# Kernel tuning notes

Measured on AMD Instinct MI355X. Metric: run time of the kernel, lower is better.

Reference implementation:

```python
import jax, jax.numpy as jnp
import numpy as np

B, N = 128, 64
HID, MLP, DS, DV = 128, 128, 32, 32
DH = MLP - DS - DV  # 64
FILL = -10.0


def _embed_mask(x, W, b, fill):
    # Linear+ReLU on non-NaN rows; fill NaN rows with `fill` (matches embed_with_masking).
    nan = jnp.isnan(x).any(-1)
    e = jax.nn.relu(jnp.where(jnp.isnan(x), 0.0, x) @ W + b)
    return jnp.where(nan[..., None], jnp.asarray(fill, x.dtype), e)


def setup_inputs() -> dict:
    key = jax.random.key(0)
    ks = jax.random.split(key, 12)
    s = 0.05
    return {
        "hidden_states": jax.random.normal(ks[0], (B, N, HID), jnp.float32),
        "obs1": jax.random.normal(ks[1], (B, N, 2), jnp.float32),
        "obs2": jax.random.normal(ks[2], (B, N, 2), jnp.float32),
        "w_sp": jax.random.normal(ks[3], (2, DS), jnp.float32) * s,
        "b_sp": jnp.zeros((DS,), jnp.float32),
        "w_vel": jax.random.normal(ks[4], (2, DV), jnp.float32) * s,
        "b_vel": jnp.zeros((DV,), jnp.float32),
        "w_hid": jax.random.normal(ks[5], (HID, DH), jnp.float32) * s,
        "b_hid": jnp.zeros((DH,), jnp.float32),
        "wq": jax.random.normal(ks[6], (MLP, MLP), jnp.float32) * s,
        "wk": jax.random.normal(ks[7], (MLP, MLP), jnp.float32) * s,
        "wv": jax.random.normal(ks[8], (MLP, MLP), jnp.float32) * s,
        "in_proj_w": jax.random.normal(ks[9], (MLP, 3 * MLP), jnp.float32) * s,
        "in_proj_b": jnp.zeros((3 * MLP,), jnp.float32),
        "mha_out_w": jax.random.normal(ks[10], (MLP, MLP), jnp.float32) * s,
        "mha_out_b": jnp.zeros((MLP,), jnp.float32),
        "out_w": jax.random.normal(ks[11], (MLP, MLP), jnp.float32) * s,
        "out_b": jnp.zeros((MLP,), jnp.float32),
    }


def reference(hidden_states, obs1, obs2, w_sp, b_sp, w_vel, b_vel, w_hid, b_hid,
              wq, wk, wv, in_proj_w, in_proj_b, mha_out_w, mha_out_b, out_w, out_b):
    b, n = obs2.shape[0], obs2.shape[1]
    # relative positions: rel[b,i,j] = obs2[b,j] - obs2[b,i]
    rel = obs2[:, None, :, :] - obs2[:, :, None, :]              # [B,N,N,2]
    sp = _embed_mask(rel, w_sp, b_sp, FILL)                      # [B,N,N,DS]
    hid = _embed_mask(hidden_states, w_hid, b_hid, 0.0)          # [B,N,DH]
    hid_unf = jnp.broadcast_to(hid[:, None, :, :], (b, n, n, DH))
    vel = obs2 - obs1
    relvel = vel[:, None, :, :] - vel[:, :, None, :]             # [B,N,N,2]
    dv = _embed_mask(relvel * 4, w_vel, b_vel, FILL)             # [B,N,N,DV]
    emb = jnp.concatenate([sp, hid_unf, dv], axis=-1)            # [B,N,N,MLP]

    # MHA (1 head) in-proj weights split (stored as [in,out])
    w_iq, w_ik, w_iv = in_proj_w[:, :MLP], in_proj_w[:, MLP:2 * MLP], in_proj_w[:, 2 * MLP:]
    b_iq, b_ik, b_iv = in_proj_b[:MLP], in_proj_b[MLP:2 * MLP], in_proj_b[2 * MLP:]

    # Only the diagonal query position is kept by the final eye-mask gather,
    # and softmax rows are independent, so compute q only at j == i.
    idx = jnp.arange(n)
    emb_diag = emb[:, idx, idx]                                  # [B,N,MLP]
    q = (emb_diag @ wq) @ w_iq + b_iq                            # [B,N,MLP]
    k = (emb @ wk) @ w_ik + b_ik                                 # [B,N,N,MLP]
    v = (emb @ wv) @ w_iv + b_iv                                 # [B,N,N,MLP]

    scores = jnp.einsum('bid,bijd->bij', q, k) / jnp.sqrt(jnp.asarray(MLP, q.dtype))
    attn = jax.nn.softmax(scores, axis=-1)                       # [B,N,N]
    ctx = jnp.einsum('bij,bijd->bid', attn, v)                   # [B,N,MLP]
    mha_out = ctx @ mha_out_w + mha_out_b
    out = mha_out @ out_w + out_b                                # [B,N,out_dim]
    return out.reshape(b * n, -1)
```

## Files before the change

kernel.cpp:

```cpp
#include <hip/hip_runtime.h>

typedef float v2f __attribute__((ext_vector_type(2)));
#define PKFMA(a,b,c) __builtin_elementwise_fma((a),(b),(c))
#define PKMAX(a,b)   __builtin_elementwise_max((a),(b))
static __device__ __forceinline__ v2f vsplat(float s) { return (v2f){s, s}; }
static __device__ __forceinline__ v2f vmk(float a, float b) { return (v2f){a, b}; }
static __device__ __forceinline__ v2f shfl_xor_v2(v2f x, int m) {
    double d = __builtin_bit_cast(double, x);
    d = __shfl_xor(d, m, 64);
    return __builtin_bit_cast(v2f, d);
}

#define WS_WQC   0
#define WS_WKC   16384
#define WS_WVC   32768
#define WS_MOW   49152
#define WS_GQ    65536
#define WS_G0Q   73728
#define WS_FALL  73856
#define WS_FB    90240
#define WS_HID   90368
#define WS_NEED_HID_BYTES ((size_t)(90368 + 128*64*64) * 4)

__global__ __launch_bounds__(256) void precompute1(
    const float* __restrict__ wq, const float* __restrict__ wk,
    const float* __restrict__ wv, const float* __restrict__ in_proj_w,
    const float* __restrict__ mha_out_w, const float* __restrict__ out_w,
    const float* __restrict__ hs, const float* __restrict__ w_hid,
    const float* __restrict__ b_hid, float* __restrict__ ws)
{
    __shared__ __align__(16) float sbuf[4224];
    const int tid = threadIdx.x;

    if (blockIdx.x < 256) {
        const int mat  = blockIdx.x >> 6;
        const int rp   = blockIdx.x & 63;
        const int rsel = tid >> 7;
        const int col  = tid & 127;
        const int r    = 2 * rp + rsel;
        const float* A; const float* Bm; int ldb; float* C;
        if (mat == 0)      { A = wq;        Bm = in_proj_w;       ldb = 384; C = ws + WS_WQC; }
        else if (mat == 1) { A = wk;        Bm = in_proj_w + 128; ldb = 384; C = ws + WS_WKC; }
        else if (mat == 2) { A = wv;        Bm = in_proj_w + 256; ldb = 384; C = ws + WS_WVC; }
        else               { A = mha_out_w; Bm = out_w;           ldb = 128; C = ws + WS_MOW; }
        sbuf[tid] = A[r * 128 + col];
        __syncthreads();
        float acc = 0.f;
        #pragma unroll 8
        for (int d = 0; d < 128; ++d) acc = fmaf(sbuf[rsel * 128 + d], Bm[d * ldb + col], acc);
        C[r * 128 + col] = acc;
    } else {
        const int b2 = blockIdx.x - 256;
        const int b = b2 >> 1, half = b2 & 1;
        const float4* src = (const float4*)(hs + b * 8192 + half * 4096);
        for (int k = tid; k < 1024; k += 256) {
            const int row = k >> 5, c = k & 31;
            *(float4*)&sbuf[row * 132 + 4 * c] = src[k];
        }
        __syncthreads();
        const int ty = tid >> 4, tx = tid & 15;
        float a0c[4] = {0,0,0,0}, a1c[4] = {0,0,0,0};
        for (int d0 = 0; d0 < 128; d0 += 4) {
            const float4 a0 = *(const float4*)&sbuf[(2*ty+0)*132 + d0];
            const float4 a1 = *(const float4*)&sbuf[(2*ty+1)*132 + d0];
            const float* a0p = (const float*)&a0;
            const float* a1p = (const float*)&a1;
            #pragma unroll
            for (int dd = 0; dd < 4; ++dd) {
                const float4 w4 = *(const float4*)&w_hid[(d0+dd)*64 + 4*tx];
                a0c[0] = fmaf(a0p[dd], w4.x, a0c[0]); a0c[1] = fmaf(a0p[dd], w4.y, a0c[1]);
                a0c[2] = fmaf(a0p[dd], w4.z, a0c[2]); a0c[3] = fmaf(a0p[dd], w4.w, a0c[3]);
                a1c[0] = fmaf(a1p[dd], w4.x, a1c[0]); a1c[1] = fmaf(a1p[dd], w4.y, a1c[1]);
                a1c[2] = fmaf(a1p[dd], w4.z, a1c[2]); a1c[3] = fmaf(a1p[dd], w4.w, a1c[3]);
            }
        }
        const float4 bh = *(const float4*)&b_hid[4*tx];
        float* dst = ws + WS_HID + b * 4096 + (32*half + 2*ty) * 64 + 4*tx;
        *(float4*)dst        = make_float4(fmaxf(a0c[0]+bh.x,0.f), fmaxf(a0c[1]+bh.y,0.f),
                                           fmaxf(a0c[2]+bh.z,0.f), fmaxf(a0c[3]+bh.w,0.f));
        *(float4*)(dst + 64) = make_float4(fmaxf(a1c[0]+bh.x,0.f), fmaxf(a1c[1]+bh.y,0.f),
                                           fmaxf(a1c[2]+bh.z,0.f), fmaxf(a1c[3]+bh.w,0.f));
    }
}

__global__ __launch_bounds__(128) void precompute2(
    const float* __restrict__ b_sp, const float* __restrict__ b_vel,
    const float* __restrict__ in_proj_b, const float* __restrict__ mha_out_b,
    const float* __restrict__ out_w, const float* __restrict__ out_b,
    float* __restrict__ ws)
{
    const float* Wqc = ws + WS_WQC;
    const float* Wkc = ws + WS_WKC;
    const float* Wvc = ws + WS_WVC;
    const float* Mow = ws + WS_MOW;
    const int bid = blockIdx.x, tid = threadIdx.x;
    __shared__ float sa[128];

    if (bid < 64) {
        const int k = bid;
        sa[tid] = Wqc[(32 + k) * 128 + tid];
        __syncthreads();
        const int j = tid;
        const int pj = (j < 64) ? 32 + j : ((j < 96) ? j - 64 : j);
        const float* brow = Wkc + pj * 128;
        float acc = 0.f;
        #pragma unroll 8
        for (int d = 0; d < 128; ++d) acc = fmaf(sa[d], brow[d], acc);
        ws[WS_GQ + k * 128 + j] = acc;
    } else if (bid < 192) {
        const int k2 = bid - 64;
        const int srcRow = (k2 < 32) ? k2 : ((k2 < 64) ? 96 + (k2 - 32) : 32 + (k2 - 64));
        sa[tid] = Wvc[srcRow * 128 + tid];
        __syncthreads();
        float acc = 0.f;
        #pragma unroll 8
        for (int m = 0; m < 128; ++m) acc = fmaf(sa[m], Mow[m * 128 + tid], acc);
        ws[WS_FALL + k2 * 128 + tid] = acc;
    } else if (bid == 192) {
        float acc = out_b[tid];
        #pragma unroll 8
        for (int m = 0; m < 128; ++m) {
            acc = fmaf(in_proj_b[256 + m], Mow[m * 128 + tid], acc);
            acc = fmaf(mha_out_b[m], out_w[m * 128 + tid], acc);
        }
        ws[WS_FB + tid] = acc;
    } else {
        float qc = in_proj_b[tid];
        #pragma unroll 4
        for (int s = 0; s < 32; ++s) {
            qc = fmaf(fmaxf(b_sp[s], 0.f),  Wqc[s * 128 + tid], qc);
            qc = fmaf(fmaxf(b_vel[s], 0.f), Wqc[(96 + s) * 128 + tid], qc);
        }
        sa[tid] = qc;
        __syncthreads();
        const int j = tid;
        const int pj = (j < 64) ? 32 + j : ((j < 96) ? j - 64 : j);
        const float* brow = Wkc + pj * 128;
        float acc = 0.f;
        #pragma unroll 8
        for (int d = 0; d < 128; ++d) acc = fmaf(sa[d], brow[d], acc);
        ws[WS_G0Q + j] = acc;
    }
}

#define L_OBS  4224
#define L_WV   4480

template <bool HIDWS>
__global__ __launch_bounds__(256) void attn_main(
    const float* __restrict__ hs, const float* __restrict__ obs1,
    const float* __restrict__ obs2,
    const float* __restrict__ w_sp, const float* __restrict__ b_sp,
    const float* __restrict__ w_vel, const float* __restrict__ b_vel,
    const float* __restrict__ w_hid, const float* __restrict__ b_hid,
    const float* __restrict__ ws, float* __restrict__ out)
{
    const int tid = threadIdx.x;
    const int l   = tid & 63;
    const int w   = tid >> 6;
    const int b   = blockIdx.x >> 2;
    const int i0  = (blockIdx.x & 3) * 16;
    const int rg0 = i0 + 4 * w;

    const float* GQ   = ws + WS_GQ;
    const float* g0q  = ws + WS_G0Q;
    const float* Fall = ws + WS_FALL;
    const float* fbv  = ws + WS_FB;

    __shared__ __align__(16) float smem[7552];
    float* const s_hid = smem;
    float* const s_obs = smem + L_OBS;
    float* const tt = smem + L_WV + w * 768;
    float* const qq = smem + L_WV + w * 768 + 256;
    float* const aa = smem + L_WV + w * 768 + 512;

    if (tid < 64) {
        const int g = b * 64 + tid;
        const float2 o2 = ((const float2*)obs2)[g];
        const float2 o1 = ((const float2*)obs1)[g];
        *(float4*)&s_obs[tid * 4] = make_float4(o2.x, o2.y, o2.x - o1.x, o2.y - o1.y);
    }
    if (HIDWS) {
        const float4* src = (const float4*)(ws + WS_HID + b * 4096);
        #pragma unroll
        for (int k = tid; k < 1024; k += 256) {
            const int row = k >> 4, c4 = (k & 15) * 4;
            const float4 v = src[k];
            *(v2f*)&s_hid[row * 66 + c4]     = vmk(v.x, v.y);
            *(v2f*)&s_hid[row * 66 + c4 + 2] = vmk(v.z, v.w);
        }
    } else {
        const int r = tid >> 2, qseg = (tid & 3) * 16;
        float acc[16];
        #pragma unroll
        for (int c = 0; c < 16; ++c) acc[c] = b_hid[qseg + c];
        for (int k = 0; k < 128; ++k) {
            const float a = hs[b * 8192 + r * 128 + k];
            #pragma unroll
            for (int c4 = 0; c4 < 4; ++c4) {
                const float4 w4 = *(const float4*)&w_hid[k * 64 + qseg + 4 * c4];
                acc[4*c4+0] = fmaf(a, w4.x, acc[4*c4+0]);
                acc[4*c4+1] = fmaf(a, w4.y, acc[4*c4+1]);
                acc[4*c4+2] = fmaf(a, w4.z, acc[4*c4+2]);
                acc[4*c4+3] = fmaf(a, w4.w, acc[4*c4+3]);
            }
        }
        #pragma unroll
        for (int c = 0; c < 16; c += 2)
            *(v2f*)&s_hid[r * 66 + qseg + c] =
                vmk(fmaxf(acc[c], 0.f), fmaxf(acc[c+1], 0.f));
    }
    __syncthreads();

    {
        const v2f bias = *(const v2f*)&g0q[2 * l];
        v2f acc0 = bias, acc1 = bias, acc2 = bias, acc3 = bias;
        for (int k0 = 0; k0 < 64; k0 += 2) {
            const v2f g0 = *(const v2f*)&GQ[k0 * 128 + 2 * l];
            const v2f g1 = *(const v2f*)&GQ[(k0 + 1) * 128 + 2 * l];
            const v2f h0 = *(const v2f*)&s_hid[(rg0 + 0) * 66 + k0];
            const v2f h1 = *(const v2f*)&s_hid[(rg0 + 1) * 66 + k0];
            const v2f h2 = *(const v2f*)&s_hid[(rg0 + 2) * 66 + k0];
            const v2f h3 = *(const v2f*)&s_hid[(rg0 + 3) * 66 + k0];
            acc0 = PKFMA(vsplat(h0.x), g0, PKFMA(vsplat(h0.y), g1, acc0));
            acc1 = PKFMA(vsplat(h1.x), g0, PKFMA(vsplat(h1.y), g1, acc1));
            acc2 = PKFMA(vsplat(h2.x), g0, PKFMA(vsplat(h2.y), g1, acc2));
            acc3 = PKFMA(vsplat(h3.x), g0, PKFMA(vsplat(h3.y), g1, acc3));
        }
        if (l < 32) {
            const int c = 2 * l;
            *(v2f*)&tt[0 * 64 + c] = acc0;  *(v2f*)&tt[1 * 64 + c] = acc1;
            *(v2f*)&tt[2 * 64 + c] = acc2;  *(v2f*)&tt[3 * 64 + c] = acc3;
        } else {
            const int c = 2 * l - 64;
            *(v2f*)&qq[0 * 64 + c] = acc0;  *(v2f*)&qq[1 * 64 + c] = acc1;
            *(v2f*)&qq[2 * 64 + c] = acc2;  *(v2f*)&qq[3 * 64 + c] = acc3;
        }
    }

    float sc[4];
    {
        v2f s0 = (v2f){0.f,0.f}, s1 = s0, s2 = s0, s3 = s0;
        const float* hl = &s_hid[l * 66];
        for (int c0 = 0; c0 < 64; c0 += 2) {
            const v2f h2 = *(const v2f*)&hl[c0];
            s0 = PKFMA(*(const v2f*)&tt[0 * 64 + c0], h2, s0);
            s1 = PKFMA(*(const v2f*)&tt[1 * 64 + c0], h2, s1);
            s2 = PKFMA(*(const v2f*)&tt[2 * 64 + c0], h2, s2);
            s3 = PKFMA(*(const v2f*)&tt[3 * 64 + c0], h2, s3);
        }
        sc[0] = s0.x + s0.y; sc[1] = s1.x + s1.y;
        sc[2] = s2.x + s2.y; sc[3] = s3.x + s3.y;
    }

    {
        const float4 oj = *(const float4*)&s_obs[4 * l];
        float rx[4], ry[4], dx[4], dy[4];
        #pragma unroll
        for (int r = 0; r < 4; ++r) {
            const float4 oi = *(const float4*)&s_obs[4 * (rg0 + r)];
            rx[r] = oj.x - oi.x;  ry[r] = oj.y - oi.y;
            dx[r] = (oj.z - oi.z) * 4.f;  dy[r] = (oj.w - oi.w) * 4.f;
        }
        v2f acc[4] = {{0,0},{0,0},{0,0},{0,0}};
        for (int s0 = 0; s0 < 32; s0 += 2) {
            const v2f w0p = *(const v2f*)&w_sp[s0];
            const v2f w1p = *(const v2f*)&w_sp[32 + s0];
            const v2f bsp = *(const v2f*)&b_sp[s0];
            const v2f u0p = *(const v2f*)&w_vel[s0];
            const v2f u1p = *(const v2f*)&w_vel[32 + s0];
            const v2f bvp = *(const v2f*)&b_vel[s0];
            #pragma unroll
            for (int r = 0; r < 4; ++r) {
                const v2f qs2 = *(const v2f*)&qq[r * 64 + s0];
                const v2f qd2 = *(const v2f*)&qq[r * 64 + 32 + s0];
                const v2f esp = PKMAX(PKFMA(vsplat(rx[r]), w0p,
                                     PKFMA(vsplat(ry[r]), w1p, bsp)), vsplat(0.f));
                acc[r] = PKFMA(qs2, esp, acc[r]);
                const v2f edv = PKMAX(PKFMA(vsplat(dx[r]), u0p,
                                     PKFMA(vsplat(dy[r]), u1p, bvp)), vsplat(0.f));
                acc[r] = PKFMA(qd2, edv, acc[r]);
            }
        }
        const float scale = 0.08838834764831845f;
        v2f p01 = vmk((sc[0] + acc[0].x + acc[0].y) * scale,
                      (sc[1] + acc[1].x + acc[1].y) * scale);
        v2f p23 = vmk((sc[2] + acc[2].x + acc[2].y) * scale,
                      (sc[3] + acc[3].x + acc[3].y) * scale);
        v2f m01 = p01, m23 = p23;
        #pragma unroll
        for (int off = 32; off > 0; off >>= 1) {
            m01 = PKMAX(m01, shfl_xor_v2(m01, off));
            m23 = PKMAX(m23, shfl_xor_v2(m23, off));
        }
        v2f e01 = vmk(__expf(p01.x - m01.x), __expf(p01.y - m01.y));
        v2f e23 = vmk(__expf(p23.x - m23.x), __expf(p23.y - m23.y));
        v2f u01 = e01, u23 = e23;
        #pragma unroll
        for (int off = 32; off > 0; off >>= 1) {
            u01 = u01 + shfl_xor_v2(u01, off);
            u23 = u23 + shfl_xor_v2(u23, off);
        }
        *(float4*)&aa[4 * l] = make_float4(e01.x / u01.x, e01.y / u01.y,
                                           e23.x / u23.x, e23.y / u23.y);
    }

    {
        const int r = l >> 4, s = l & 15;
        const v2f w0p = vmk(w_sp[s],        w_sp[s + 16]);
        const v2f w1p = vmk(w_sp[32 + s],   w_sp[48 + s]);
        const v2f bsp = vmk(b_sp[s],        b_sp[s + 16]);
        const v2f u0p = vmk(w_vel[s],       w_vel[s + 16]);
        const v2f u1p = vmk(w_vel[32 + s],  w_vel[48 + s]);
        const v2f bvp = vmk(b_vel[s],       b_vel[s + 16]);
        const float4 oi = *(const float4*)&s_obs[4 * (rg0 + r)];
        v2f asp = (v2f){0.f, 0.f}, adv = asp;
        for (int j = 0; j < 64; ++j) {
            const float a = aa[4 * j + r];
            const float4 o4 = *(const float4*)&s_obs[4 * j];
            const float rxx = o4.x - oi.x, ryy = o4.y - oi.y;
            const float dxx = (o4.z - oi.z) * 4.f, dyy = (o4.w - oi.w) * 4.f;
            const v2f esp = PKMAX(PKFMA(vsplat(rxx), w0p,
                                 PKFMA(vsplat(ryy), w1p, bsp)), vsplat(0.f));
            asp = PKFMA(vsplat(a), esp, asp);
            const v2f edv = PKMAX(PKFMA(vsplat(dxx), u0p,
                                 PKFMA(vsplat(dyy), u1p, bvp)), vsplat(0.f));
            adv = PKFMA(vsplat(a), edv, adv);
        }
        tt[r * 64 + s]      = asp.x;
        tt[r * 64 + s + 16] = asp.y;
        tt[r * 64 + 32 + s] = adv.x;
        tt[r * 64 + 48 + s] = adv.y;
    }

    {
        float ah0 = 0.f, ah1 = 0.f, ah2 = 0.f, ah3 = 0.f;
        for (int j = 0; j < 64; j += 2) {
            const float4 a0 = *(const float4*)&aa[4 * j];
            const float4 a1 = *(const float4*)&aa[4 * j + 4];
            const float h0 = s_hid[j * 66 + l];
            const float h1 = s_hid[(j + 1) * 66 + l];
            ah0 = fmaf(a0.x, h0, fmaf(a1.x, h1, ah0));
            ah1 = fmaf(a0.y, h0, fmaf(a1.y, h1, ah1));
            ah2 = fmaf(a0.z, h0, fmaf(a1.z, h1, ah2));
            ah3 = fmaf(a0.w, h0, fmaf(a1.w, h1, ah3));
        }
        qq[0 * 64 + l] = ah0;  qq[1 * 64 + l] = ah1;
        qq[2 * 64 + l] = ah2;  qq[3 * 64 + l] = ah3;
    }

    {
        const v2f fb2 = *(const v2f*)&fbv[2 * l];
        v2f o0 = fb2, o1 = fb2, o2 = fb2, o3 = fb2;
        for (int k = 0; k < 64; k += 2) {
            const v2f f0 = *(const v2f*)&Fall[k * 128 + 2 * l];
            const v2f f1 = *(const v2f*)&Fall[(k + 1) * 128 + 2 * l];
            const v2f A0 = *(const v2f*)&tt[0 * 64 + k];
            const v2f A1 = *(const v2f*)&tt[1 * 64 + k];
            const v2f A2 = *(const v2f*)&tt[2 * 64 + k];
            const v2f A3 = *(const v2f*)&tt[3 * 64 + k];
            o0 = PKFMA(vsplat(A0.x), f0, PKFMA(vsplat(A0.y), f1, o0));
            o1 = PKFMA(vsplat(A1.x), f0, PKFMA(vsplat(A1.y), f1, o1));
            o2 = PKFMA(vsplat(A2.x), f0, PKFMA(vsplat(A2.y), f1, o2));
            o3 = PKFMA(vsplat(A3.x), f0, PKFMA(vsplat(A3.y), f1, o3));
        }
        for (int k = 0; k < 64; k += 2) {
            const v2f f0 = *(const v2f*)&Fall[(64 + k) * 128 + 2 * l];
            const v2f f1 = *(const v2f*)&Fall[(65 + k) * 128 + 2 * l];
            const v2f A0 = *(const v2f*)&qq[0 * 64 + k];
            const v2f A1 = *(const v2f*)&qq[1 * 64 + k];
            const v2f A2 = *(const v2f*)&qq[2 * 64 + k];
            const v2f A3 = *(const v2f*)&qq[3 * 64 + k];
            o0 = PKFMA(vsplat(A0.x), f0, PKFMA(vsplat(A0.y), f1, o0));
            o1 = PKFMA(vsplat(A1.x), f0, PKFMA(vsplat(A1.y), f1, o1));
            o2 = PKFMA(vsplat(A2.x), f0, PKFMA(vsplat(A2.y), f1, o2));
            o3 = PKFMA(vsplat(A3.x), f0, PKFMA(vsplat(A3.y), f1, o3));
        }
        const int gr = (b * 64 + rg0) * 128 + 2 * l;
        *(v2f*)&out[gr]           = o0;
        *(v2f*)&out[gr + 128]     = o1;
        *(v2f*)&out[gr + 256]     = o2;
        *(v2f*)&out[gr + 384]     = o3;
    }
}

extern "C" void kernel_launch(void* const* d_in, const int* in_sizes, int n_in,
                              void* d_out, int out_size, void* d_ws, size_t ws_size,
                              hipStream_t stream) {
    const float* hs        = (const float*)d_in[0];
    const float* obs1      = (const float*)d_in[1];
    const float* obs2      = (const float*)d_in[2];
    const float* w_sp      = (const float*)d_in[3];
    const float* b_sp      = (const float*)d_in[4];
    const float* w_vel     = (const float*)d_in[5];
    const float* b_vel     = (const float*)d_in[6];
    const float* w_hid     = (const float*)d_in[7];
    const float* b_hid     = (const float*)d_in[8];
    const float* wq        = (const float*)d_in[9];
    const float* wk        = (const float*)d_in[10];
    const float* wv        = (const float*)d_in[11];
    const float* in_proj_w = (const float*)d_in[12];
    const float* in_proj_b = (const float*)d_in[13];
    const float* mha_out_w = (const float*)d_in[14];
    const float* mha_out_b = (const float*)d_in[15];
    const float* out_w     = (const float*)d_in[16];
    const float* out_b     = (const float*)d_in[17];
    float* ws  = (float*)d_ws;
    float* out = (float*)d_out;

    const bool hidws = (ws_size >= WS_NEED_HID_BYTES);

    precompute1<<<hidws ? 512 : 256, 256, 0, stream>>>(
        wq, wk, wv, in_proj_w, mha_out_w, out_w, hs, w_hid, b_hid, ws);
    precompute2<<<194, 128, 0, stream>>>(
        b_sp, b_vel, in_proj_b, mha_out_b, out_w, out_b, ws);
    if (hidws) {
        attn_main<true><<<512, 256, 0, stream>>>(hs, obs1, obs2, w_sp, b_sp, w_vel, b_vel,
                                                 w_hid, b_hid, ws, out);
    } else {
        attn_main<false><<<512, 256, 0, stream>>>(hs, obs1, obs2, w_sp, b_sp, w_vel, b_vel,
                                                  w_hid, b_hid, ws, out);
    }
}
```

Before: 128.9 us.

## Halve rows per wave in attn_main and vectorize precompute2 dot products

The attention kernel now gives each wave 2 query rows instead of 4 and launches 1024 blocks instead of 512, with shared-memory scratch resized to match. The context accumulation is rearranged so each lane handles one (row, feature) pair that packs the spatial and velocity embeddings into a single v2f. This is meant to spread the work over more CUs on the MI355X and shorten each block's serial chain. The cost is reloading the per-batch hidden and obs data in twice as many blocks and less reuse of the GQ/Fall loads across rows. Separately, precompute2's dot products now read float4 at a time.

```diff
diff --git a/kernel.cpp b/kernel.cpp
--- a/kernel.cpp
+++ b/kernel.cpp
@@ -94,7 +94,7 @@
     const float* Wvc = ws + WS_WVC;
     const float* Mow = ws + WS_MOW;
     const int bid = blockIdx.x, tid = threadIdx.x;
-    __shared__ float sa[128];
+    __shared__ __align__(16) float sa[128];
 
     if (bid < 64) {
         const int k = bid;
@@ -105,7 +105,11 @@
         const float* brow = Wkc + pj * 128;
         float acc = 0.f;
         #pragma unroll 8
-        for (int d = 0; d < 128; ++d) acc = fmaf(sa[d], brow[d], acc);
+        for (int d = 0; d < 128; d += 4) {
+            const float4 a4 = *(const float4*)&sa[d];
+            const float4 b4 = *(const float4*)&brow[d];
+            acc = fmaf(a4.x, b4.x, fmaf(a4.y, b4.y, fmaf(a4.z, b4.z, fmaf(a4.w, b4.w, acc))));
+        }
         ws[WS_GQ + k * 128 + j] = acc;
     } else if (bid < 192) {
         const int k2 = bid - 64;
@@ -138,7 +142,11 @@
         const float* brow = Wkc + pj * 128;
         float acc = 0.f;
         #pragma unroll 8
-        for (int d = 0; d < 128; ++d) acc = fmaf(sa[d], brow[d], acc);
+        for (int d = 0; d < 128; d += 4) {
+            const float4 a4 = *(const float4*)&sa[d];
+            const float4 b4 = *(const float4*)&brow[d];
+            acc = fmaf(a4.x, b4.x, fmaf(a4.y, b4.y, fmaf(a4.z, b4.z, fmaf(a4.w, b4.w, acc))));
+        }
         ws[WS_G0Q + j] = acc;
     }
 }
@@ -158,21 +166,21 @@
     const int tid = threadIdx.x;
     const int l   = tid & 63;
     const int w   = tid >> 6;
-    const int b   = blockIdx.x >> 2;
-    const int i0  = (blockIdx.x & 3) * 16;
-    const int rg0 = i0 + 4 * w;
+    const int b   = blockIdx.x >> 3;
+    const int i0  = (blockIdx.x & 7) * 8;
+    const int rg0 = i0 + 2 * w;
 
     const float* GQ   = ws + WS_GQ;
     const float* g0q  = ws + WS_G0Q;
     const float* Fall = ws + WS_FALL;
     const float* fbv  = ws + WS_FB;
 
-    __shared__ __align__(16) float smem[7552];
+    __shared__ __align__(16) float smem[6016];
     float* const s_hid = smem;
     float* const s_obs = smem + L_OBS;
-    float* const tt = smem + L_WV + w * 768;
-    float* const qq = smem + L_WV + w * 768 + 256;
-    float* const aa = smem + L_WV + w * 768 + 512;
+    float* const tt = smem + L_WV + w * 384;
+    float* const qq = smem + L_WV + w * 384 + 128;
+    float* const aa = smem + L_WV + w * 384 + 256;
 
     if (tid < 64) {
         const int g = b * 64 + tid;
@@ -214,55 +222,48 @@
 
     {
         const v2f bias = *(const v2f*)&g0q[2 * l];
-        v2f acc0 = bias, acc1 = bias, acc2 = bias, acc3 = bias;
+        v2f acc0 = bias, acc1 = bias;
         for (int k0 = 0; k0 < 64; k0 += 2) {
             const v2f g0 = *(const v2f*)&GQ[k0 * 128 + 2 * l];
             const v2f g1 = *(const v2f*)&GQ[(k0 + 1) * 128 + 2 * l];
             const v2f h0 = *(const v2f*)&s_hid[(rg0 + 0) * 66 + k0];
             const v2f h1 = *(const v2f*)&s_hid[(rg0 + 1) * 66 + k0];
-            const v2f h2 = *(const v2f*)&s_hid[(rg0 + 2) * 66 + k0];
-            const v2f h3 = *(const v2f*)&s_hid[(rg0 + 3) * 66 + k0];
             acc0 = PKFMA(vsplat(h0.x), g0, PKFMA(vsplat(h0.y), g1, acc0));
             acc1 = PKFMA(vsplat(h1.x), g0, PKFMA(vsplat(h1.y), g1, acc1));
-            acc2 = PKFMA(vsplat(h2.x), g0, PKFMA(vsplat(h2.y), g1, acc2));
-            acc3 = PKFMA(vsplat(h3.x), g0, PKFMA(vsplat(h3.y), g1, acc3));
         }
         if (l < 32) {
             const int c = 2 * l;
-            *(v2f*)&tt[0 * 64 + c] = acc0;  *(v2f*)&tt[1 * 64 + c] = acc1;
-            *(v2f*)&tt[2 * 64 + c] = acc2;  *(v2f*)&tt[3 * 64 + c] = acc3;
+            *(v2f*)&tt[c]      = acc0;
+            *(v2f*)&tt[64 + c] = acc1;
         } else {
             const int c = 2 * l - 64;
-            *(v2f*)&qq[0 * 64 + c] = acc0;  *(v2f*)&qq[1 * 64 + c] = acc1;
-            *(v2f*)&qq[2 * 64 + c] = acc2;  *(v2f*)&qq[3 * 64 + c] = acc3;
-        }
-    }
-
-    float sc[4];
-    {
-        v2f s0 = (v2f){0.f,0.f}, s1 = s0, s2 = s0, s3 = s0;
+            *(v2f*)&qq[c]      = acc0;
+            *(v2f*)&qq[64 + c] = acc1;
+        }
+    }
+
+    float sc0, sc1;
+    {
+        v2f s0 = (v2f){0.f,0.f}, s1 = s0;
         const float* hl = &s_hid[l * 66];
         for (int c0 = 0; c0 < 64; c0 += 2) {
             const v2f h2 = *(const v2f*)&hl[c0];
-            s0 = PKFMA(*(const v2f*)&tt[0 * 64 + c0], h2, s0);
-            s1 = PKFMA(*(const v2f*)&tt[1 * 64 + c0], h2, s1);
-            s2 = PKFMA(*(const v2f*)&tt[2 * 64 + c0], h2, s2);
-            s3 = PKFMA(*(const v2f*)&tt[3 * 64 + c0], h2, s3);
-        }
-        sc[0] = s0.x + s0.y; sc[1] = s1.x + s1.y;
-        sc[2] = s2.x + s2.y; sc[3] = s3.x + s3.y;
-    }
-
-    {
-        const float4 oj = *(const float4*)&s_obs[4 * l];
-        float rx[4], ry[4], dx[4], dy[4];
-        #pragma unroll
-        for (int r = 0; r < 4; ++r) {
-            const float4 oi = *(const float4*)&s_obs[4 * (rg0 + r)];
-            rx[r] = oj.x - oi.x;  ry[r] = oj.y - oi.y;
-            dx[r] = (oj.z - oi.z) * 4.f;  dy[r] = (oj.w - oi.w) * 4.f;
-        }
-        v2f acc[4] = {{0,0},{0,0},{0,0},{0,0}};
+            s0 = PKFMA(*(const v2f*)&tt[c0],      h2, s0);
+            s1 = PKFMA(*(const v2f*)&tt[64 + c0], h2, s1);
+        }
+        sc0 = s0.x + s0.y;
+        sc1 = s1.x + s1.y;
+    }
+
+    {
+        const float4 oj  = *(const float4*)&s_obs[4 * l];
+        const float4 oiA = *(const float4*)&s_obs[4 * rg0];
+        const float4 oiB = *(const float4*)&s_obs[4 * (rg0 + 1)];
+        const float rxA = oj.x - oiA.x, ryA = oj.y - oiA.y;
+        const float dxA = (oj.z - oiA.z) * 4.f, dyA = (oj.w - oiA.w) * 4.f;
+        const float rxB = oj.x - oiB.x, ryB = oj.y - oiB.y;
+        const float dxB = (oj.z - oiB.z) * 4.f, dyB = (oj.w - oiB.w) * 4.f;
+        v2f accA = (v2f){0.f, 0.f}, accB = accA;
         for (int s0 = 0; s0 < 32; s0 += 2) {
             const v2f w0p = *(const v2f*)&w_sp[s0];
             const v2f w1p = *(const v2f*)&w_sp[32 + s0];
@@ -270,117 +271,85 @@
             const v2f u0p = *(const v2f*)&w_vel[s0];
             const v2f u1p = *(const v2f*)&w_vel[32 + s0];
             const v2f bvp = *(const v2f*)&b_vel[s0];
-            #pragma unroll
-            for (int r = 0; r < 4; ++r) {
-                const v2f qs2 = *(const v2f*)&qq[r * 64 + s0];
-                const v2f qd2 = *(const v2f*)&qq[r * 64 + 32 + s0];
-                const v2f esp = PKMAX(PKFMA(vsplat(rx[r]), w0p,
-                                     PKFMA(vsplat(ry[r]), w1p, bsp)), vsplat(0.f));
-                acc[r] = PKFMA(qs2, esp, acc[r]);
-                const v2f edv = PKMAX(PKFMA(vsplat(dx[r]), u0p,
-                                     PKFMA(vsplat(dy[r]), u1p, bvp)), vsplat(0.f));
-                acc[r] = PKFMA(qd2, edv, acc[r]);
-            }
+            const v2f qsA = *(const v2f*)&qq[s0];
+            const v2f qsB = *(const v2f*)&qq[64 + s0];
+            const v2f qdA = *(const v2f*)&qq[32 + s0];
+            const v2f qdB = *(const v2f*)&qq[96 + s0];
+            const v2f espA = PKMAX(PKFMA(vsplat(rxA), w0p, PKFMA(vsplat(ryA), w1p, bsp)), vsplat(0.f));
+            const v2f edvA = PKMAX(PKFMA(vsplat(dxA), u0p, PKFMA(vsplat(dyA), u1p, bvp)), vsplat(0.f));
+            accA = PKFMA(qsA, espA, PKFMA(qdA, edvA, accA));
+            const v2f espB = PKMAX(PKFMA(vsplat(rxB), w0p, PKFMA(vsplat(ryB), w1p, bsp)), vsplat(0.f));
+            const v2f edvB = PKMAX(PKFMA(vsplat(dxB), u0p, PKFMA(vsplat(dyB), u1p, bvp)), vsplat(0.f));
+            accB = PKFMA(qsB, espB, PKFMA(qdB, edvB, accB));
         }
         const float scale = 0.08838834764831845f;
-        v2f p01 = vmk((sc[0] + acc[0].x + acc[0].y) * scale,
-                      (sc[1] + acc[1].x + acc[1].y) * scale);
-        v2f p23 = vmk((sc[2] + acc[2].x + acc[2].y) * scale,
-                      (sc[3] + acc[3].x + acc[3].y) * scale);
-        v2f m01 = p01, m23 = p23;
-        #pragma unroll
-        for (int off = 32; off > 0; off >>= 1) {
-            m01 = PKMAX(m01, shfl_xor_v2(m01, off));
-            m23 = PKMAX(m23, shfl_xor_v2(m23, off));
-        }
-        v2f e01 = vmk(__expf(p01.x - m01.x), __expf(p01.y - m01.y));
-        v2f e23 = vmk(__expf(p23.x - m23.x), __expf(p23.y - m23.y));
-        v2f u01 = e01, u23 = e23;
-        #pragma unroll
-        for (int off = 32; off > 0; off >>= 1) {
-            u01 = u01 + shfl_xor_v2(u01, off);
-            u23 = u23 + shfl_xor_v2(u23, off);
-        }
-        *(float4*)&aa[4 * l] = make_float4(e01.x / u01.x, e01.y / u01.y,
-                                           e23.x / u23.x, e23.y / u23.y);
-    }
-
-    {
-        const int r = l >> 4, s = l & 15;
-        const v2f w0p = vmk(w_sp[s],        w_sp[s + 16]);
-        const v2f w1p = vmk(w_sp[32 + s],   w_sp[48 + s]);
-        const v2f bsp = vmk(b_sp[s],        b_sp[s + 16]);
-        const v2f u0p = vmk(w_vel[s],       w_vel[s + 16]);
-        const v2f u1p = vmk(w_vel[32 + s],  w_vel[48 + s]);
-        const v2f bvp = vmk(b_vel[s],       b_vel[s + 16]);
+        v2f p = vmk((sc0 + accA.x + accA.y) * scale,
+                    (sc1 + accB.x + accB.y) * scale);
+        v2f m = p;
+        #pragma unroll
+        for (int off = 32; off > 0; off >>= 1) m = PKMAX(m, shfl_xor_v2(m, off));
+        v2f e = vmk(__expf(p.x - m.x), __expf(p.y - m.y));
+        v2f u = e;
+        #pragma unroll
+        for (int off = 32; off > 0; off >>= 1) u = u + shfl_xor_v2(u, off);
+        *(v2f*)&aa[2 * l] = vmk(e.x / u.x, e.y / u.y);
+    }
+
+    {
+        const int r = l >> 5, s = l & 31;
+        const v2f w0p = vmk(w_sp[s],      w_vel[s]);
+        const v2f w1p = vmk(w_sp[32 + s], w_vel[32 + s]);
+        const v2f bp  = vmk(b_sp[s],      b_vel[s]);
         const float4 oi = *(const float4*)&s_obs[4 * (rg0 + r)];
-        v2f asp = (v2f){0.f, 0.f}, adv = asp;
+        v2f acc = (v2f){0.f, 0.f};
         for (int j = 0; j < 64; ++j) {
-            const float a = aa[4 * j + r];
+            const float a = aa[2 * j + r];
             const float4 o4 = *(const float4*)&s_obs[4 * j];
-            const float rxx = o4.x - oi.x, ryy = o4.y - oi.y;
-            const float dxx = (o4.z - oi.z) * 4.f, dyy = (o4.w - oi.w) * 4.f;
-            const v2f esp = PKMAX(PKFMA(vsplat(rxx), w0p,
-                                 PKFMA(vsplat(ryy), w1p, bsp)), vsplat(0.f));
-            asp = PKFMA(vsplat(a), esp, asp);
-            const v2f edv = PKMAX(PKFMA(vsplat(dxx), u0p,
-                                 PKFMA(vsplat(dyy), u1p, bvp)), vsplat(0.f));
-            adv = PKFMA(vsplat(a), edv, adv);
-        }
-        tt[r * 64 + s]      = asp.x;
-        tt[r * 64 + s + 16] = asp.y;
-        tt[r * 64 + 32 + s] = adv.x;
-        tt[r * 64 + 48 + s] = adv.y;
-    }
-
-    {
-        float ah0 = 0.f, ah1 = 0.f, ah2 = 0.f, ah3 = 0.f;
+            const float rx = o4.x - oi.x, ry = o4.y - oi.y;
+            const float dx = (o4.z - oi.z) * 4.f, dy = (o4.w - oi.w) * 4.f;
+            const v2f uv = PKMAX(PKFMA(vmk(rx, dx), w0p,
+                                 PKFMA(vmk(ry, dy), w1p, bp)), vsplat(0.f));
+            acc = PKFMA(vsplat(a), uv, acc);
+        }
+        tt[r * 64 + s]      = acc.x;
+        tt[r * 64 + 32 + s] = acc.y;
+    }
+
+    {
+        float ah0 = 0.f, ah1 = 0.f;
         for (int j = 0; j < 64; j += 2) {
-            const float4 a0 = *(const float4*)&aa[4 * j];
-            const float4 a1 = *(const float4*)&aa[4 * j + 4];
+            const float4 a2 = *(const float4*)&aa[2 * j];
             const float h0 = s_hid[j * 66 + l];
             const float h1 = s_hid[(j + 1) * 66 + l];
-            ah0 = fmaf(a0.x, h0, fmaf(a1.x, h1, ah0));
-            ah1 = fmaf(a0.y, h0, fmaf(a1.y, h1, ah1));
-            ah2 = fmaf(a0.z, h0, fmaf(a1.z, h1, ah2));
-            ah3 = fmaf(a0.w, h0, fmaf(a1.w, h1, ah3));
-        }
-        qq[0 * 64 + l] = ah0;  qq[1 * 64 + l] = ah1;
-        qq[2 * 64 + l] = ah2;  qq[3 * 64 + l] = ah3;
+            ah0 = fmaf(a2.x, h0, fmaf(a2.z, h1, ah0));
+            ah1 = fmaf(a2.y, h0, fmaf(a2.w, h1, ah1));
+        }
+        qq[l]      = ah0;
+        qq[64 + l] = ah1;
     }
 
     {
         const v2f fb2 = *(const v2f*)&fbv[2 * l];
-        v2f o0 = fb2, o1 = fb2, o2 = fb2, o3 = fb2;
+        v2f o0 = fb2, o1 = fb2;
         for (int k = 0; k < 64; k += 2) {
             const v2f f0 = *(const v2f*)&Fall[k * 128 + 2 * l];
             const v2f f1 = *(const v2f*)&Fall[(k + 1) * 128 + 2 * l];
-            const v2f A0 = *(const v2f*)&tt[0 * 64 + k];
-            const v2f A1 = *(const v2f*)&tt[1 * 64 + k];
-            const v2f A2 = *(const v2f*)&tt[2 * 64 + k];
-            const v2f A3 = *(const v2f*)&tt[3 * 64 + k];
+            const v2f A0 = *(const v2f*)&tt[k];
+            const v2f A1 = *(const v2f*)&tt[64 + k];
             o0 = PKFMA(vsplat(A0.x), f0, PKFMA(vsplat(A0.y), f1, o0));
             o1 = PKFMA(vsplat(A1.x), f0, PKFMA(vsplat(A1.y), f1, o1));
-            o2 = PKFMA(vsplat(A2.x), f0, PKFMA(vsplat(A2.y), f1, o2));
-            o3 = PKFMA(vsplat(A3.x), f0, PKFMA(vsplat(A3.y), f1, o3));
         }
         for (int k = 0; k < 64; k += 2) {
             const v2f f0 = *(const v2f*)&Fall[(64 + k) * 128 + 2 * l];
             const v2f f1 = *(const v2f*)&Fall[(65 + k) * 128 + 2 * l];
-            const v2f A0 = *(const v2f*)&qq[0 * 64 + k];
-            const v2f A1 = *(const v2f*)&qq[1 * 64 + k];
-            const v2f A2 = *(const v2f*)&qq[2 * 64 + k];
-            const v2f A3 = *(const v2f*)&qq[3 * 64 + k];
+            const v2f A0 = *(const v2f*)&qq[k];
+            const v2f A1 = *(const v2f*)&qq[64 + k];
             o0 = PKFMA(vsplat(A0.x), f0, PKFMA(vsplat(A0.y), f1, o0));
             o1 = PKFMA(vsplat(A1.x), f0, PKFMA(vsplat(A1.y), f1, o1));
-            o2 = PKFMA(vsplat(A2.x), f0, PKFMA(vsplat(A2.y), f1, o2));
-            o3 = PKFMA(vsplat(A3.x), f0, PKFMA(vsplat(A3.y), f1, o3));
         }
         const int gr = (b * 64 + rg0) * 128 + 2 * l;
-        *(v2f*)&out[gr]           = o0;
-        *(v2f*)&out[gr + 128]     = o1;
-        *(v2f*)&out[gr + 256]     = o2;
-        *(v2f*)&out[gr + 384]     = o3;
+        *(v2f*)&out[gr]       = o0;
+        *(v2f*)&out[gr + 128] = o1;
     }
 }
 
@@ -415,10 +384,10 @@
     precompute2<<<194, 128, 0, stream>>>(
         b_sp, b_vel, in_proj_b, mha_out_b, out_w, out_b, ws);
     if (hidws) {
-        attn_main<true><<<512, 256, 0, stream>>>(hs, obs1, obs2, w_sp, b_sp, w_vel, b_vel,
-                                                 w_hid, b_hid, ws, out);
+        attn_main<true><<<1024, 256, 0, stream>>>(hs, obs1, obs2, w_sp, b_sp, w_vel, b_vel,
+                                                  w_hid, b_hid, ws, out);
     } else {
-        attn_main<false><<<512, 256, 0, stream>>>(hs, obs1, obs2, w_sp, b_sp, w_vel, b_vel,
-                                                  w_hid, b_hid, ws, out);
-    }
-}
+        attn_main<false><<<1024, 256, 0, stream>>>(hs, obs1, obs2, w_sp, b_sp, w_vel, b_vel,
+                                                   w_hid, b_hid, ws, out);
+    }
+}
```

Result: slower. 140.5 us (+9.0%).
